# Kernel tuning notes

Hardware: AMD Instinct MI355X
Metric: run time of the kernel (lower is better)

## Reference

```python
import jax, jax.numpy as jnp
import numpy as np

B, D, U, M, K = 8192, 512, 512, 16, 64


def setup_inputs() -> dict:
    key = jax.random.key(0)
    ks = jax.random.split(key, 5)
    return {
        "x": jax.random.normal(ks[0], (B, D), dtype=jnp.float32),
        "key_kernel": jax.random.normal(ks[1], (D, K), dtype=jnp.float32) * (1.0 / np.sqrt(D)),
        "key_bias": jnp.zeros((K,), dtype=jnp.float32),
        "keys_map": jax.random.normal(ks[2], (M, K), dtype=jnp.float32),
        "kernels": jax.random.normal(ks[3], (M, D, U), dtype=jnp.float32) * (1.0 / np.sqrt(D)),
        "biases": jnp.zeros((M, U), dtype=jnp.float32),
    }


def reference(x, key_kernel, key_bias, keys_map, kernels, biases):
    # key projection: [B, K]
    keyv = x @ key_kernel + key_bias
    # inverse-distance similarity to mode keys: [B, M]
    dist = jnp.sqrt(jnp.sum((keyv[:, None, :] - keys_map[None, :, :]) ** 2, axis=-1))
    sim = 1.0 / (dist + 1.0)
    modes = kernels.shape[0]
    # kernel = mean_m(sim_m * kernels_m); out = x @ kernel.
    # Distributive identity: out = (1/M) * sum_m sim_m * (x @ kernels_m)
    out = jnp.einsum("bm,bd,mdu->bu", sim, x, kernels) / modes
    # bias = mean_m(sim_m * biases_m): [B, U]
    out = out + (sim @ biases) / modes
    return out
```

## Files before the change

### kernel.cpp

```cpp
#include <hip/hip_runtime.h>
#include <hip/hip_bf16.h>
#include <stdint.h>

#define B_SZ 8192
#define D_SZ 512
#define U_SZ 512
#define M_SZ 16
#define K_SZ 64

typedef short bf16x8 __attribute__((ext_vector_type(8)));
typedef float f32x4 __attribute__((ext_vector_type(4)));

__device__ __forceinline__ unsigned short f2bf(float f) {
  union { float f; unsigned u; } v; v.f = f;
  unsigned r = v.u + 0x7fffu + ((v.u >> 16) & 1u);
  return (unsigned short)(r >> 16);
}

__global__ __launch_bounds__(256) void prep1(
    const float* __restrict__ x, const float* __restrict__ key_kernel,
    const float* __restrict__ kernels, unsigned short* __restrict__ xbf,
    unsigned short* __restrict__ kbf, unsigned short* __restrict__ wkbf) {
  __shared__ float tf[32][65];
  int bid = blockIdx.x;
  int t = threadIdx.x;

  if (bid < 2048) {
    int m = bid >> 7;
    int rem = bid & 127;
    int a = (rem >> 3) & 15;
    int ut = rem & 7;
    int d0 = a * 32, u0 = ut * 64;
    {
      int dr = t >> 4, uc = t & 15;
      const float* src = kernels + ((size_t)m * D_SZ + d0 + dr) * U_SZ + u0 + uc * 4;
      float4 aa = *(const float4*)src;
      float4 bb = *(const float4*)(src + (size_t)16 * U_SZ);
      tf[dr][uc * 4 + 0] = aa.x; tf[dr][uc * 4 + 1] = aa.y;
      tf[dr][uc * 4 + 2] = aa.z; tf[dr][uc * 4 + 3] = aa.w;
      tf[dr + 16][uc * 4 + 0] = bb.x; tf[dr + 16][uc * 4 + 1] = bb.y;
      tf[dr + 16][uc * 4 + 2] = bb.z; tf[dr + 16][uc * 4 + 3] = bb.w;
    }
    __syncthreads();
    {
      int ur = t >> 2, dc = t & 3;
      int j = ur >> 4, lane16 = ur & 15;
      int kt = a >> 1, h = a & 1;
      unsigned short* dst = kbf +
          (((((size_t)m * 8 + ut) * 8 + kt) * 4 + j) * 2 + h) * 512 +
          ((size_t)dc * 16 + lane16) * 8;
      ushort4 lo, hi;
      lo.x = f2bf(tf[dc * 8 + 0][ur]); lo.y = f2bf(tf[dc * 8 + 1][ur]);
      lo.z = f2bf(tf[dc * 8 + 2][ur]); lo.w = f2bf(tf[dc * 8 + 3][ur]);
      hi.x = f2bf(tf[dc * 8 + 4][ur]); hi.y = f2bf(tf[dc * 8 + 5][ur]);
      hi.z = f2bf(tf[dc * 8 + 6][ur]); hi.w = f2bf(tf[dc * 8 + 7][ur]);
      *(ushort4*)dst = lo;
      *(ushort4*)(dst + 4) = hi;
    }
    return;
  }

  if (bid < 2056) {
    int kt = bid - 2048;
#pragma unroll
    for (int rep = 0; rep < 2; ++rep) {
      int c = rep * 256 + t;
      int j = c >> 7, h = (c >> 6) & 1, quad = (c >> 4) & 3, ln = c & 15;
      int dd = kt * 64 + h * 32 + quad * 8;
      int u = j * 16 + ln;
      unsigned short v[8];
#pragma unroll
      for (int e = 0; e < 8; ++e)
        v[e] = f2bf(key_kernel[(size_t)(dd + e) * K_SZ + u]);
      unsigned short* dst =
          wkbf + ((size_t)((kt * 4 + j) * 2 + h) * 64 + quad * 16 + ln) * 8;
#pragma unroll
      for (int e = 0; e < 8; ++e) dst[e] = v[e];
    }
    return;
  }

  int xb0 = bid - 2056;
  int bt = xb0 >> 3, i = xb0 & 7;
  int b0 = xb0 * 16;
#pragma unroll
  for (int rep = 0; rep < 4; ++rep) {
    int idx = rep * 256 + t;
    int kt = idx >> 7, h = (idx >> 6) & 1, quad = (idx >> 4) & 3, ln = idx & 15;
    const float* src = x + (size_t)(b0 + ln) * D_SZ + kt * 64 + h * 32 + quad * 8;
    float4 a = *(const float4*)src;
    float4 b = *(const float4*)(src + 4);
    ushort4 lo, hi;
    lo.x = f2bf(a.x); lo.y = f2bf(a.y); lo.z = f2bf(a.z); lo.w = f2bf(a.w);
    hi.x = f2bf(b.x); hi.y = f2bf(b.y); hi.z = f2bf(b.z); hi.w = f2bf(b.w);
    unsigned short* dst =
        xbf + ((((size_t)bt * 8 + kt) * 8 + i) * 2 + h) * 512 +
        ((size_t)quad * 16 + ln) * 8;
    *(ushort4*)dst = lo;
    *(ushort4*)(dst + 4) = hi;
  }
}

__global__ __launch_bounds__(256) void prep2(
    const unsigned short* __restrict__ xbf, const unsigned short* __restrict__ wkbf,
    const float* __restrict__ key_bias, const float* __restrict__ keys_map,
    float* __restrict__ simT) {
  __shared__ float kv[64][68];
  __shared__ float sKM[16][64];
  int t = threadIdx.x, w = t >> 6, l = t & 63;
  int blk = blockIdx.x;
  int b0 = blk * 64, bt = blk >> 1, ibase = (blk & 1) * 4;
  int lane16 = l & 15, quad = l >> 4;

  ((float4*)sKM)[t] = ((const float4*)keys_map)[t];

  f32x4 acc[4];
#pragma unroll
  for (int j = 0; j < 4; ++j) acc[j] = (f32x4){0.f, 0.f, 0.f, 0.f};

  for (int kt = 0; kt < 8; ++kt) {
    bf16x8 af[2];
#pragma unroll
    for (int h = 0; h < 2; ++h)
      af[h] = *(const bf16x8*)(xbf +
                               ((((size_t)bt * 8 + kt) * 8 + ibase + w) * 2 + h) * 512 +
                               (size_t)l * 8);
#pragma unroll
    for (int j = 0; j < 4; ++j) {
      bf16x8 b0f = *(const bf16x8*)(wkbf + ((size_t)((kt * 4 + j) * 2 + 0) * 64 + l) * 8);
      bf16x8 b1f = *(const bf16x8*)(wkbf + ((size_t)((kt * 4 + j) * 2 + 1) * 64 + l) * 8);
      acc[j] = __builtin_amdgcn_mfma_f32_16x16x32_bf16(af[0], b0f, acc[j], 0, 0, 0);
      acc[j] = __builtin_amdgcn_mfma_f32_16x16x32_bf16(af[1], b1f, acc[j], 0, 0, 0);
    }
  }
#pragma unroll
  for (int j = 0; j < 4; ++j) {
    float bc = key_bias[j * 16 + lane16];
#pragma unroll
    for (int r = 0; r < 4; ++r)
      kv[w * 16 + quad * 4 + r][j * 16 + lane16] = acc[j][r] + bc;
  }
  __syncthreads();

  int row = t >> 2, mg = (t & 3) * 4;
  float d2[4] = {0.f, 0.f, 0.f, 0.f};
#pragma unroll 8
  for (int k = 0; k < 64; ++k) {
    float kvv = kv[row][k];
#pragma unroll
    for (int q = 0; q < 4; ++q) {
      float df = kvv - sKM[mg + q][k];
      d2[q] += df * df;
    }
  }
#pragma unroll
  for (int q = 0; q < 4; ++q)
    simT[(size_t)(mg + q) * B_SZ + b0 + row] = 1.0f / (sqrtf(d2[q]) + 1.0f);
}

__global__ __launch_bounds__(256, 2) void poly_gemm(
    const unsigned short* __restrict__ xbf,
    const unsigned short* __restrict__ kbf,
    const float* __restrict__ simT,
    const float* __restrict__ biases,
    float* __restrict__ out) {
  __shared__ float sRed[8192];

  int t = threadIdx.x, w = t >> 6, l = t & 63;
  int bid = blockIdx.x;
  int ut = bid & 7, bt = bid >> 3;
  int b0 = bt * 128, u0 = ut * 64;
  int half = w >> 1, rw = w & 1;
  int lane16 = l & 15, quad = l >> 4;

  f32x4 facc[4][4];
#pragma unroll
  for (int i = 0; i < 4; ++i)
#pragma unroll
    for (int j = 0; j < 4; ++j) facc[i][j] = (f32x4){0.f, 0.f, 0.f, 0.f};

#pragma unroll 1
  for (int kt = 0; kt < 8; ++kt) {
    bf16x8 af[4][2];
#pragma unroll
    for (int ii = 0; ii < 4; ++ii)
#pragma unroll
      for (int h = 0; h < 2; ++h)
        af[ii][h] = *(const bf16x8*)(
            xbf + ((((size_t)bt * 8 + kt) * 8 + rw * 4 + ii) * 2 + h) * 512 +
            (size_t)l * 8);

#pragma unroll 2
    for (int mi = 0; mi < 8; ++mi) {
      int mode = half * 8 + mi;
      const unsigned short* bb =
          kbf + ((((size_t)mode * 8 + ut) * 8 + kt) * 4) * 2 * 512;
      bf16x8 bfr[4][2];
#pragma unroll
      for (int j = 0; j < 4; ++j)
#pragma unroll
        for (int h = 0; h < 2; ++h)
          bfr[j][h] = *(const bf16x8*)(bb + ((size_t)(j * 2 + h)) * 512 +
                                       (size_t)l * 8);

      f32x4 sv[4];
#pragma unroll
      for (int i = 0; i < 4; ++i)
        sv[i] = *(const f32x4*)(simT + (size_t)mode * B_SZ + b0 + rw * 64 +
                                i * 16 + quad * 4);

#pragma unroll
      for (int i = 0; i < 4; ++i)
#pragma unroll
        for (int j = 0; j < 4; ++j) {
          f32x4 p = __builtin_amdgcn_mfma_f32_16x16x32_bf16(
              af[i][0], bfr[j][0], (f32x4){0.f, 0.f, 0.f, 0.f}, 0, 0, 0);
          p = __builtin_amdgcn_mfma_f32_16x16x32_bf16(af[i][1], bfr[j][1], p,
                                                      0, 0, 0);
#pragma unroll
          for (int r = 0; r < 4; ++r) facc[i][j][r] += sv[i][r] * p[r];
        }

      if (kt == 0) {
        float bbv[4];
#pragma unroll
        for (int j = 0; j < 4; ++j)
          bbv[j] = biases[(size_t)mode * U_SZ + u0 + j * 16 + lane16];
#pragma unroll
        for (int i = 0; i < 4; ++i)
#pragma unroll
          for (int j = 0; j < 4; ++j)
#pragma unroll
            for (int r = 0; r < 4; ++r) facc[i][j][r] += sv[i][r] * bbv[j];
      }
    }
  }

  __syncthreads();
  if (half == 1) {
#pragma unroll
    for (int i = 0; i < 4; ++i)
#pragma unroll
      for (int r = 0; r < 4; ++r)
#pragma unroll
        for (int j = 0; j < 4; ++j)
          sRed[rw * 4096 + (i * 16 + quad * 4 + r) * 64 + j * 16 + lane16] =
              facc[i][j][r];
  }
  __syncthreads();
  if (half == 0) {
#pragma unroll
    for (int i = 0; i < 4; ++i)
#pragma unroll
      for (int r = 0; r < 4; ++r) {
        int row = b0 + rw * 64 + i * 16 + quad * 4 + r;
        float* orow = out + (size_t)row * U_SZ + u0;
#pragma unroll
        for (int j = 0; j < 4; ++j)
          orow[j * 16 + lane16] =
              (facc[i][j][r] +
               sRed[rw * 4096 + (i * 16 + quad * 4 + r) * 64 + j * 16 + lane16]) *
              0.0625f;
      }
  }
}

extern "C" void kernel_launch(void* const* d_in, const int* in_sizes, int n_in,
                              void* d_out, int out_size, void* d_ws, size_t ws_size,
                              hipStream_t stream) {
  const float* x = (const float*)d_in[0];
  const float* key_kernel = (const float*)d_in[1];
  const float* key_bias = (const float*)d_in[2];
  const float* keys_map = (const float*)d_in[3];
  const float* kernels = (const float*)d_in[4];
  const float* biases = (const float*)d_in[5];
  float* out = (float*)d_out;

  char* p = (char*)d_ws;
  unsigned short* xbf = (unsigned short*)p;  p += (size_t)B_SZ * D_SZ * 2;
  unsigned short* kbf = (unsigned short*)p;  p += (size_t)M_SZ * U_SZ * D_SZ * 2;
  unsigned short* wkbf = (unsigned short*)p; p += (size_t)K_SZ * D_SZ * 2;
  float* simT = (float*)p;

  prep1<<<dim3(2568), 256, 0, stream>>>(x, key_kernel, kernels, xbf, kbf, wkbf);
  prep2<<<dim3(128), 256, 0, stream>>>(xbf, wkbf, key_bias, keys_map, simT);
  poly_gemm<<<dim3(512), 256, 0, stream>>>(xbf, kbf, simT, biases, out);
}
```

Baseline: 172.6 us.

## Fuse key projection and similarity into GEMM, halve output tile width

```diff
diff --git a/kernel.cpp b/kernel.cpp
--- a/kernel.cpp
+++ b/kernel.cpp
@@ -29,8 +29,8 @@
     int m = bid >> 7;
     int rem = bid & 127;
     int a = (rem >> 3) & 15;
-    int ut = rem & 7;
-    int d0 = a * 32, u0 = ut * 64;
+    int ut64 = rem & 7;
+    int d0 = a * 32, u0 = ut64 * 64;
     {
       int dr = t >> 4, uc = t & 15;
       const float* src = kernels + ((size_t)m * D_SZ + d0 + dr) * U_SZ + u0 + uc * 4;
@@ -44,10 +44,12 @@
     __syncthreads();
     {
       int ur = t >> 2, dc = t & 3;
-      int j = ur >> 4, lane16 = ur & 15;
       int kt = a >> 1, h = a & 1;
+      int ut16 = ut64 * 2 + (ur >> 5);
+      int j2 = (ur >> 4) & 1;
+      int lane16 = ur & 15;
       unsigned short* dst = kbf +
-          (((((size_t)m * 8 + ut) * 8 + kt) * 4 + j) * 2 + h) * 512 +
+          (((((size_t)m * 16 + ut16) * 8 + kt) * 2 + j2) * 2 + h) * 512 +
           ((size_t)dc * 16 + lane16) * 8;
       ushort4 lo, hi;
       lo.x = f2bf(tf[dc * 8 + 0][ur]); lo.y = f2bf(tf[dc * 8 + 1][ur]);
@@ -101,83 +103,95 @@
   }
 }
 
-__global__ __launch_bounds__(256) void prep2(
-    const unsigned short* __restrict__ xbf, const unsigned short* __restrict__ wkbf,
-    const float* __restrict__ key_bias, const float* __restrict__ keys_map,
-    float* __restrict__ simT) {
-  __shared__ float kv[64][68];
-  __shared__ float sKM[16][64];
-  int t = threadIdx.x, w = t >> 6, l = t & 63;
-  int blk = blockIdx.x;
-  int b0 = blk * 64, bt = blk >> 1, ibase = (blk & 1) * 4;
-  int lane16 = l & 15, quad = l >> 4;
-
-  ((float4*)sKM)[t] = ((const float4*)keys_map)[t];
-
-  f32x4 acc[4];
-#pragma unroll
-  for (int j = 0; j < 4; ++j) acc[j] = (f32x4){0.f, 0.f, 0.f, 0.f};
-
-  for (int kt = 0; kt < 8; ++kt) {
-    bf16x8 af[2];
-#pragma unroll
-    for (int h = 0; h < 2; ++h)
-      af[h] = *(const bf16x8*)(xbf +
-                               ((((size_t)bt * 8 + kt) * 8 + ibase + w) * 2 + h) * 512 +
-                               (size_t)l * 8);
-#pragma unroll
-    for (int j = 0; j < 4; ++j) {
-      bf16x8 b0f = *(const bf16x8*)(wkbf + ((size_t)((kt * 4 + j) * 2 + 0) * 64 + l) * 8);
-      bf16x8 b1f = *(const bf16x8*)(wkbf + ((size_t)((kt * 4 + j) * 2 + 1) * 64 + l) * 8);
-      acc[j] = __builtin_amdgcn_mfma_f32_16x16x32_bf16(af[0], b0f, acc[j], 0, 0, 0);
-      acc[j] = __builtin_amdgcn_mfma_f32_16x16x32_bf16(af[1], b1f, acc[j], 0, 0, 0);
-    }
-  }
-#pragma unroll
-  for (int j = 0; j < 4; ++j) {
-    float bc = key_bias[j * 16 + lane16];
-#pragma unroll
-    for (int r = 0; r < 4; ++r)
-      kv[w * 16 + quad * 4 + r][j * 16 + lane16] = acc[j][r] + bc;
-  }
-  __syncthreads();
-
-  int row = t >> 2, mg = (t & 3) * 4;
-  float d2[4] = {0.f, 0.f, 0.f, 0.f};
-#pragma unroll 8
-  for (int k = 0; k < 64; ++k) {
-    float kvv = kv[row][k];
-#pragma unroll
-    for (int q = 0; q < 4; ++q) {
-      float df = kvv - sKM[mg + q][k];
-      d2[q] += df * df;
-    }
-  }
-#pragma unroll
-  for (int q = 0; q < 4; ++q)
-    simT[(size_t)(mg + q) * B_SZ + b0 + row] = 1.0f / (sqrtf(d2[q]) + 1.0f);
-}
-
-__global__ __launch_bounds__(256, 2) void poly_gemm(
+__global__ __launch_bounds__(256, 4) void poly_gemm(
     const unsigned short* __restrict__ xbf,
     const unsigned short* __restrict__ kbf,
-    const float* __restrict__ simT,
-    const float* __restrict__ biases,
-    float* __restrict__ out) {
-  __shared__ float sRed[8192];
+    const unsigned short* __restrict__ wkbf,
+    const float* __restrict__ key_bias, const float* __restrict__ keys_map,
+    const float* __restrict__ biases, float* __restrict__ out) {
+  __shared__ float smem[128 * 68];
 
   int t = threadIdx.x, w = t >> 6, l = t & 63;
   int bid = blockIdx.x;
-  int ut = bid & 7, bt = bid >> 3;
-  int b0 = bt * 128, u0 = ut * 64;
+  int ut = bid & 15, bt = bid >> 4;
+  int b0 = bt * 128, u0 = ut * 32;
+  int lane16 = l & 15, quad = l >> 4;
+
+  {
+    f32x4 acc[2][4];
+#pragma unroll
+    for (int ii = 0; ii < 2; ++ii)
+#pragma unroll
+      for (int j = 0; j < 4; ++j) acc[ii][j] = (f32x4){0.f, 0.f, 0.f, 0.f};
+    for (int kt = 0; kt < 8; ++kt) {
+      bf16x8 af[2][2];
+#pragma unroll
+      for (int ii = 0; ii < 2; ++ii)
+#pragma unroll
+        for (int h = 0; h < 2; ++h)
+          af[ii][h] = *(const bf16x8*)(
+              xbf + ((((size_t)bt * 8 + kt) * 8 + w * 2 + ii) * 2 + h) * 512 +
+              (size_t)l * 8);
+#pragma unroll
+      for (int j = 0; j < 4; ++j) {
+        bf16x8 bw0 = *(const bf16x8*)(wkbf + ((size_t)((kt * 4 + j) * 2 + 0)) * 512 + (size_t)l * 8);
+        bf16x8 bw1 = *(const bf16x8*)(wkbf + ((size_t)((kt * 4 + j) * 2 + 1)) * 512 + (size_t)l * 8);
+#pragma unroll
+        for (int ii = 0; ii < 2; ++ii) {
+          acc[ii][j] = __builtin_amdgcn_mfma_f32_16x16x32_bf16(af[ii][0], bw0, acc[ii][j], 0, 0, 0);
+          acc[ii][j] = __builtin_amdgcn_mfma_f32_16x16x32_bf16(af[ii][1], bw1, acc[ii][j], 0, 0, 0);
+        }
+      }
+    }
+#pragma unroll
+    for (int j = 0; j < 4; ++j) {
+      float bc = key_bias[j * 16 + lane16];
+#pragma unroll
+      for (int ii = 0; ii < 2; ++ii)
+#pragma unroll
+        for (int r = 0; r < 4; ++r)
+          smem[(w * 32 + ii * 16 + quad * 4 + r) * 68 + j * 16 + lane16] =
+              acc[ii][j][r] + bc;
+    }
+  }
+  __syncthreads();
+
+  {
+    int row = t >> 1, kh = t & 1;
+    float kvr[32];
+#pragma unroll
+    for (int q = 0; q < 8; ++q) {
+      float4 v = *(const float4*)&smem[row * 68 + kh * 32 + q * 4];
+      kvr[q * 4 + 0] = v.x; kvr[q * 4 + 1] = v.y;
+      kvr[q * 4 + 2] = v.z; kvr[q * 4 + 3] = v.w;
+    }
+    __syncthreads();
+    float part[16];
+#pragma unroll
+    for (int m = 0; m < 16; ++m) {
+      float d2 = 0.f;
+#pragma unroll
+      for (int k = 0; k < 32; ++k) {
+        float df = kvr[k] - keys_map[m * 64 + kh * 32 + k];
+        d2 += df * df;
+      }
+      part[m] = d2;
+    }
+#pragma unroll
+    for (int m = 0; m < 16; ++m) {
+      float d2 = part[m] + __shfl_xor(part[m], 1);
+      float s = 1.0f / (sqrtf(d2) + 1.0f);
+      if ((m >> 3) == kh) smem[m * 128 + row] = s;
+    }
+  }
+  __syncthreads();
+
   int half = w >> 1, rw = w & 1;
-  int lane16 = l & 15, quad = l >> 4;
-
-  f32x4 facc[4][4];
+  f32x4 facc[4][2];
 #pragma unroll
   for (int i = 0; i < 4; ++i)
 #pragma unroll
-    for (int j = 0; j < 4; ++j) facc[i][j] = (f32x4){0.f, 0.f, 0.f, 0.f};
+    for (int j = 0; j < 2; ++j) facc[i][j] = (f32x4){0.f, 0.f, 0.f, 0.f};
 
 #pragma unroll 1
   for (int kt = 0; kt < 8; ++kt) {
@@ -194,48 +208,46 @@
     for (int mi = 0; mi < 8; ++mi) {
       int mode = half * 8 + mi;
       const unsigned short* bb =
-          kbf + ((((size_t)mode * 8 + ut) * 8 + kt) * 4) * 2 * 512;
-      bf16x8 bfr[4][2];
-#pragma unroll
-      for (int j = 0; j < 4; ++j)
+          kbf + ((((size_t)mode * 16 + ut) * 8 + kt) * 2) * 2 * 512;
+      bf16x8 bfr[2][2];
+#pragma unroll
+      for (int j = 0; j < 2; ++j)
 #pragma unroll
         for (int h = 0; h < 2; ++h)
           bfr[j][h] = *(const bf16x8*)(bb + ((size_t)(j * 2 + h)) * 512 +
                                        (size_t)l * 8);
-
       f32x4 sv[4];
 #pragma unroll
       for (int i = 0; i < 4; ++i)
-        sv[i] = *(const f32x4*)(simT + (size_t)mode * B_SZ + b0 + rw * 64 +
-                                i * 16 + quad * 4);
+        sv[i] = *(const f32x4*)&smem[mode * 128 + rw * 64 + i * 16 + quad * 4];
 
 #pragma unroll
       for (int i = 0; i < 4; ++i)
 #pragma unroll
-        for (int j = 0; j < 4; ++j) {
+        for (int j = 0; j < 2; ++j) {
           f32x4 p = __builtin_amdgcn_mfma_f32_16x16x32_bf16(
               af[i][0], bfr[j][0], (f32x4){0.f, 0.f, 0.f, 0.f}, 0, 0, 0);
-          p = __builtin_amdgcn_mfma_f32_16x16x32_bf16(af[i][1], bfr[j][1], p,
-                                                      0, 0, 0);
+          p = __builtin_amdgcn_mfma_f32_16x16x32_bf16(af[i][1], bfr[j][1], p, 0, 0, 0);
 #pragma unroll
           for (int r = 0; r < 4; ++r) facc[i][j][r] += sv[i][r] * p[r];
         }
 
       if (kt == 0) {
-        float bbv[4];
-#pragma unroll
-        for (int j = 0; j < 4; ++j)
+        float bbv[2];
+#pragma unroll
+        for (int j = 0; j < 2; ++j)
           bbv[j] = biases[(size_t)mode * U_SZ + u0 + j * 16 + lane16];
 #pragma unroll
         for (int i = 0; i < 4; ++i)
 #pragma unroll
-          for (int j = 0; j < 4; ++j)
+          for (int j = 0; j < 2; ++j)
 #pragma unroll
             for (int r = 0; r < 4; ++r) facc[i][j][r] += sv[i][r] * bbv[j];
       }
     }
   }
 
+  float* sRed = smem + 2048;
   __syncthreads();
   if (half == 1) {
 #pragma unroll
@@ -243,8 +255,8 @@
 #pragma unroll
       for (int r = 0; r < 4; ++r)
 #pragma unroll
-        for (int j = 0; j < 4; ++j)
-          sRed[rw * 4096 + (i * 16 + quad * 4 + r) * 64 + j * 16 + lane16] =
+        for (int j = 0; j < 2; ++j)
+          sRed[rw * 2048 + (i * 16 + quad * 4 + r) * 32 + j * 16 + lane16] =
               facc[i][j][r];
   }
   __syncthreads();
@@ -256,10 +268,10 @@
         int row = b0 + rw * 64 + i * 16 + quad * 4 + r;
         float* orow = out + (size_t)row * U_SZ + u0;
 #pragma unroll
-        for (int j = 0; j < 4; ++j)
+        for (int j = 0; j < 2; ++j)
           orow[j * 16 + lane16] =
               (facc[i][j][r] +
-               sRed[rw * 4096 + (i * 16 + quad * 4 + r) * 64 + j * 16 + lane16]) *
+               sRed[rw * 2048 + (i * 16 + quad * 4 + r) * 32 + j * 16 + lane16]) *
               0.0625f;
       }
   }
@@ -279,10 +291,9 @@
   char* p = (char*)d_ws;
   unsigned short* xbf = (unsigned short*)p;  p += (size_t)B_SZ * D_SZ * 2;
   unsigned short* kbf = (unsigned short*)p;  p += (size_t)M_SZ * U_SZ * D_SZ * 2;
-  unsigned short* wkbf = (unsigned short*)p; p += (size_t)K_SZ * D_SZ * 2;
-  float* simT = (float*)p;
+  unsigned short* wkbf = (unsigned short*)p;
 
   prep1<<<dim3(2568), 256, 0, stream>>>(x, key_kernel, kernels, xbf, kbf, wkbf);
-  prep2<<<dim3(128), 256, 0, stream>>>(xbf, wkbf, key_bias, keys_map, simT);
-  poly_gemm<<<dim3(512), 256, 0, stream>>>(xbf, kbf, simT, biases, out);
-}
+  poly_gemm<<<dim3(1024), 256, 0, stream>>>(xbf, kbf, wkbf, key_bias, keys_map,
+                                            biases, out);
+}
```

Result: slower. 374.1 us (+116.8%).
